# Performance work log

Hardware: AMD Instinct MI355X
Metric: run time of the kernel (lower is better)

Reference implementation:

```python
import jax, jax.numpy as jnp
import numpy as np

INPUT_DIM = 1024
EMBED_DIM = 256


def setup_inputs() -> dict:
    key = jax.random.key(0)
    ks = jax.random.split(key, 7)
    s_in = 1.0 / np.sqrt(INPUT_DIM)
    x = jax.random.normal(ks[0], (4, 2048, INPUT_DIM), dtype=jnp.float32)
    Wq = jax.random.uniform(ks[1], (INPUT_DIM, EMBED_DIM), jnp.float32, -s_in, s_in)
    bq = jax.random.uniform(ks[2], (EMBED_DIM,), jnp.float32, -s_in, s_in)
    Wk = jax.random.uniform(ks[3], (INPUT_DIM, EMBED_DIM), jnp.float32, -s_in, s_in)
    bk = jax.random.uniform(ks[4], (EMBED_DIM,), jnp.float32, -s_in, s_in)
    Wv = jax.random.uniform(ks[5], (INPUT_DIM, EMBED_DIM), jnp.float32, -s_in, s_in)
    bv = jax.random.uniform(ks[6], (EMBED_DIM,), jnp.float32, -s_in, s_in)
    return {"x": x, "Wq": Wq, "bq": bq, "Wk": Wk, "bk": bk, "Wv": Wv, "bv": bv}


def reference(x, Wq, bq, Wk, bk, Wv, bv):
    # B,T,C -> single-head attention. NOTE: original multiplies by C**0.5.
    C = x.shape[-1]
    scale = jnp.asarray(C, x.dtype) ** 0.5
    q = jnp.einsum('btc,ce->bte', x, Wq) + bq  # [B,T,E]
    k = jnp.einsum('btc,ce->bte', x, Wk) + bk
    v = jnp.einsum('btc,ce->bte', x, Wv) + bv
    wei = jnp.einsum('bqe,bke->bqk', q, k) * scale  # [B,T,T]
    wei = jax.nn.softmax(wei, axis=-1)
    # dropout p=0.0 (eval): identity
    out = jnp.einsum('bqk,bke->bqe', wei, v)  # [B,T,E]
    return out
```

## Files before the change

### kernel.cpp

```cpp
#include <hip/hip_runtime.h>
#include <math.h>

#define IDIM 1024
#define EDIM 256
#define NB 4
#define NT 2048
#define NROW 8192

typedef __attribute__((ext_vector_type(8))) short short8;
typedef __attribute__((ext_vector_type(4))) float f32x4;

#define MFMA16(A,B,C) __builtin_amdgcn_mfma_f32_16x16x32_bf16(A,B,C,0,0,0)
#define GLD16(gsrc, ldst) __builtin_amdgcn_global_load_lds( \
    (const __attribute__((address_space(1))) unsigned int*)(gsrc), \
    (__attribute__((address_space(3))) unsigned int*)(ldst), 16, 0, 0)

__device__ __forceinline__ unsigned short f2bf(float x){
    unsigned u = __builtin_bit_cast(unsigned, x);
    u += 0x7fffu + ((u >> 16) & 1u);
    return (unsigned short)(u >> 16);
}
__device__ __forceinline__ float bf2f(unsigned short h){
    unsigned u = ((unsigned)h) << 16;
    return __builtin_bit_cast(float, u);
}

__global__ __launch_bounds__(256) void split_w(
    const float* __restrict__ Wq, const float* __restrict__ Wk, const float* __restrict__ Wv,
    ushort* __restrict__ Wqh, ushort* __restrict__ Wql,
    ushort* __restrict__ Wkh, ushort* __restrict__ Wkl,
    ushort* __restrict__ Wvh)
{
    int u = blockIdx.x * 256 + threadIdx.x;
    int z   = u >> 15;
    int rem = u & 32767;
    int ko  = rem >> 8;
    int e   = rem & 255;
    const float* W = (z == 0) ? Wq : (z == 1) ? Wk : Wv;
    ushort* Oh = (z == 0) ? Wqh : (z == 1) ? Wkh : Wvh;
    ushort* Ol = (z == 0) ? Wql : Wkl;
    union { ushort us[8]; uint4 v; } hi, lo;
    #pragma unroll
    for (int j = 0; j < 8; ++j) {
        float wv = W[(size_t)(ko * 8 + j) * 256 + e];
        unsigned short h = f2bf(wv);
        hi.us[j] = h;
        lo.us[j] = f2bf(wv - bf2f(h));
    }
    *(uint4*)(Oh + (size_t)e * 1024 + ko * 8) = hi.v;
    if (z < 2) *(uint4*)(Ol + (size_t)e * 1024 + ko * 8) = lo.v;
}

__global__ __launch_bounds__(256, 3) void qkv_proj(
    const float* __restrict__ X,
    const ushort* __restrict__ Whq, const ushort* __restrict__ Wlq,
    const ushort* __restrict__ Whk, const ushort* __restrict__ Wlk,
    const ushort* __restrict__ Whv,
    const float* __restrict__ bq, const float* __restrict__ bk, const float* __restrict__ bv,
    ushort* __restrict__ Qh, ushort* __restrict__ Ql,
    ushort* __restrict__ Kh, ushort* __restrict__ Kl,
    ushort* __restrict__ Vt)
{
    __shared__ ushort Ah[259 * 8], Al[259 * 8];
    __shared__ ushort Bh[512 * 8], Bl[512 * 8];

    const int tid = threadIdx.x;
    const int lane = tid & 63, w = tid >> 6;
    const int ln = tid & 15, quad = (tid >> 4) & 3;
    const int z = blockIdx.z;
    const int n0 = blockIdx.x * 128, m0 = blockIdx.y * 64;
    const ushort* Wh = (z == 0) ? Whq : (z == 1) ? Whk : Whv;
    const ushort* Wl = (z == 0) ? Wlq : Wlk;

    f32x4 acc[4][2];
    #pragma unroll
    for (int mi = 0; mi < 4; ++mi)
        #pragma unroll
        for (int ni = 0; ni < 2; ++ni) acc[mi][ni] = (f32x4){0.f, 0.f, 0.f, 0.f};

    const int am = tid >> 2, ak8 = (tid & 3) * 8;
    const float* xp = X + (size_t)(m0 + am) * IDIM + ak8;
    const ushort* bsrc0 = Wh + (size_t)(n0 + lane) * IDIM + w * 8;
    const ushort* bsrc1 = Wh + (size_t)(n0 + 64 + lane) * IDIM + w * 8;
    const ushort* blsrc0 = Wl + (size_t)(n0 + lane) * IDIM + w * 8;
    const ushort* blsrc1 = Wl + (size_t)(n0 + 64 + lane) * IDIM + w * 8;
    ushort* bd0 = Bh + (size_t)(w * 128) * 8;
    ushort* bd1 = Bh + (size_t)(w * 128 + 64) * 8;
    ushort* bld0 = Bl + (size_t)(w * 128) * 8;
    ushort* bld1 = Bl + (size_t)(w * 128 + 64) * 8;

    for (int kk = 0; kk < IDIM; kk += 32) {
        GLD16(bsrc0 + kk, bd0);
        GLD16(bsrc1 + kk, bd1);
        if (z < 2) { GLD16(blsrc0 + kk, bld0); GLD16(blsrc1 + kk, bld1); }
        {
            float4 a0 = *(const float4*)(xp + kk);
            float4 a1 = *(const float4*)(xp + kk + 4);
            float xv[8] = {a0.x, a0.y, a0.z, a0.w, a1.x, a1.y, a1.z, a1.w};
            union { ushort us[8]; uint4 v; } hi, lo;
            #pragma unroll
            for (int j = 0; j < 8; ++j) {
                unsigned short hh = f2bf(xv[j]);
                hi.us[j] = hh;
                lo.us[j] = f2bf(xv[j] - bf2f(hh));
            }
            int unit = (tid & 3) * 65 + am;
            *(uint4*)(Ah + unit * 8) = hi.v;
            if (z < 2) *(uint4*)(Al + unit * 8) = lo.v;
        }
        __syncthreads();

        short8 ah[4], al4[4];
        #pragma unroll
        for (int mi = 0; mi < 4; ++mi) {
            int au = quad * 65 + mi * 16 + ln;
            ah[mi] = *(const short8*)(Ah + au * 8);
            if (z < 2) al4[mi] = *(const short8*)(Al + au * 8);
        }
        #pragma unroll
        for (int ni = 0; ni < 2; ++ni) {
            int bu = quad * 128 + w * 32 + ni * 16 + ln;
            short8 bh = *(const short8*)(Bh + bu * 8);
            if (z < 2) {
                short8 bl = *(const short8*)(Bl + bu * 8);
                #pragma unroll
                for (int mi = 0; mi < 4; ++mi) {
                    acc[mi][ni] = MFMA16(ah[mi], bh, acc[mi][ni]);
                    acc[mi][ni] = MFMA16(ah[mi], bl, acc[mi][ni]);
                    acc[mi][ni] = MFMA16(al4[mi], bh, acc[mi][ni]);
                }
            } else {
                #pragma unroll
                for (int mi = 0; mi < 4; ++mi)
                    acc[mi][ni] = MFMA16(ah[mi], bh, acc[mi][ni]);
            }
        }
        __syncthreads();
    }

    if (z < 2) {
        ushort* OH = (z == 0) ? Qh : Kh;
        ushort* OL = (z == 0) ? Ql : Kl;
        const float* bias = (z == 0) ? bq : bk;
        const float scale = (z == 0) ? 46.16624130844683f : 1.0f;
        #pragma unroll
        for (int ni = 0; ni < 2; ++ni) {
            int col = n0 + w * 32 + ni * 16 + ln;
            float bb = bias[col];
            #pragma unroll
            for (int mi = 0; mi < 4; ++mi)
                #pragma unroll
                for (int r = 0; r < 4; ++r) {
                    int row = m0 + mi * 16 + quad * 4 + r;
                    float v = (acc[mi][ni][r] + bb) * scale;
                    unsigned short hh = f2bf(v);
                    OH[(size_t)row * EDIM + col] = hh;
                    OL[(size_t)row * EDIM + col] = f2bf(v - bf2f(hh));
                }
        }
    } else {
        #pragma unroll
        for (int ni = 0; ni < 2; ++ni) {
            int col = n0 + w * 32 + ni * 16 + ln;
            float bb = bv[col];
            #pragma unroll
            for (int mi = 0; mi < 4; ++mi) {
                int rowb = m0 + mi * 16 + quad * 4;
                union { ushort us[4]; uint2 v; } pk;
                #pragma unroll
                for (int r = 0; r < 4; ++r) pk.us[r] = f2bf(acc[mi][ni][r] + bb);
                *(uint2*)(Vt + (size_t)col * NROW + rowb) = pk.v;
            }
        }
    }
}

__global__ __launch_bounds__(256, 2) void attn(
    const ushort* __restrict__ Qh, const ushort* __restrict__ Ql,
    const ushort* __restrict__ Kh, const ushort* __restrict__ Kl,
    const ushort* __restrict__ Vt, ushort* __restrict__ Op, float* __restrict__ mlbuf)
{
    __shared__ ushort KVbuf[4096];
    __shared__ ushort Qls[16384];
    __shared__ ushort Pall[4 * 1088];

    const int tid = threadIdx.x;
    const int lane = tid & 63;
    const int ln = tid & 15, quad = (tid >> 4) & 3, w = tid >> 6;
    ushort* Qls_w = Qls + w * 4096;
    ushort* Pw = Pall + w * 1088;

    const int id = blockIdx.x;
    const int cls = id & 15;
    const int b = cls >> 2, kvq = cls & 3;
    const int qt = id >> 4;
    const int qrow0w = b * NT + qt * 64 + w * 16;
    const int kvbase = b * NT + kvq * 512;

    short8 qh8[8];
    #pragma unroll
    for (int kc = 0; kc < 8; ++kc)
        qh8[kc] = *(const short8*)(Qh + (size_t)(qrow0w + ln) * EDIM + kc * 32 + quad * 8);
    #pragma unroll
    for (int i = 0; i < 8; ++i) {
        int u = i * 64 + lane;
        int ko = u >> 4, ln2 = u & 15;
        *(uint4*)(Qls_w + u * 8) =
            *(const uint4*)(Ql + (size_t)(qrow0w + ln2) * EDIM + ko * 8);
    }

    float m_r[4], l_r[4];
    #pragma unroll
    for (int r = 0; r < 4; ++r) { m_r[r] = -3e38f; l_r[r] = 0.f; }
    f32x4 o[16];
    #pragma unroll
    for (int ni = 0; ni < 16; ++ni) o[ni] = (f32x4){0.f, 0.f, 0.f, 0.f};

    for (int t = 0; t < 8; ++t) {
        const int kv0 = kvbase + t * 64;
        f32x4 s[4];
        #pragma unroll
        for (int ni = 0; ni < 4; ++ni) s[ni] = (f32x4){0.f, 0.f, 0.f, 0.f};

        #pragma unroll
        for (int kc = 0; kc < 8; ++kc) {
            size_t goff = (size_t)(kv0 + w * 16 + (lane & 15)) * EDIM
                          + kc * 32 + (lane >> 4) * 8;
            GLD16(Kh + goff, KVbuf + w * 512);
            GLD16(Kl + goff, KVbuf + 2048 + w * 512);
            __syncthreads();
            short8 ql8 = *(const short8*)(Qls_w + ((kc * 4 + quad) * 16 + ln) * 8);
            #pragma unroll
            for (int ni = 0; ni < 4; ++ni) {
                short8 bh = *(const short8*)(KVbuf + (ni * 64 + quad * 16 + ln) * 8);
                short8 bl = *(const short8*)(KVbuf + 2048 + (ni * 64 + quad * 16 + ln) * 8);
                s[ni] = MFMA16(qh8[kc], bh, s[ni]);
                s[ni] = MFMA16(qh8[kc], bl, s[ni]);
                s[ni] = MFMA16(ql8, bh, s[ni]);
            }
            __syncthreads();
        }

        float mt[4];
        #pragma unroll
        for (int r = 0; r < 4; ++r)
            mt[r] = fmaxf(fmaxf(s[0][r], s[1][r]), fmaxf(s[2][r], s[3][r]));
        #pragma unroll
        for (int mask = 1; mask < 16; mask <<= 1)
            #pragma unroll
            for (int r = 0; r < 4; ++r)
                mt[r] = fmaxf(mt[r], __shfl_xor(mt[r], mask));
        float alpha[4];
        #pragma unroll
        for (int r = 0; r < 4; ++r) {
            float mn = fmaxf(m_r[r], mt[r]);
            alpha[r] = exp2f(m_r[r] - mn);
            m_r[r] = mn;
        }
        float ls[4] = {0.f, 0.f, 0.f, 0.f};
        #pragma unroll
        for (int ni = 0; ni < 4; ++ni) {
            int colb = ni * 16 + ln;
            #pragma unroll
            for (int r = 0; r < 4; ++r) {
                float p = exp2f(s[ni][r] - m_r[r]);
                ls[r] += p;
                Pw[((colb >> 3) * 17 + quad * 4 + r) * 8 + (colb & 7)] = f2bf(p);
            }
        }
        #pragma unroll
        for (int mask = 1; mask < 16; mask <<= 1)
            #pragma unroll
            for (int r = 0; r < 4; ++r)
                ls[r] += __shfl_xor(ls[r], mask);
        #pragma unroll
        for (int r = 0; r < 4; ++r) l_r[r] = l_r[r] * alpha[r] + ls[r];
        #pragma unroll
        for (int ni = 0; ni < 16; ++ni)
            #pragma unroll
            for (int r = 0; r < 4; ++r) o[ni][r] *= alpha[r];

        short8 apk0 = *(const short8*)(Pw + (quad * 17 + ln) * 8);
        short8 apk1 = *(const short8*)(Pw + ((4 + quad) * 17 + ln) * 8);
        #pragma unroll
        for (int vs = 0; vs < 4; ++vs) {
            size_t gv = (size_t)(vs * 64 + w * 16 + (lane & 15)) * NROW
                        + kv0 + (lane >> 4) * 8;
            GLD16(Vt + gv, KVbuf + w * 1024);
            GLD16(Vt + gv + 32, KVbuf + w * 1024 + 512);
            __syncthreads();
            #pragma unroll
            for (int ni = 0; ni < 4; ++ni) {
                short8 v0 = *(const short8*)(KVbuf + (ni * 128 + quad * 16 + ln) * 8);
                short8 v1 = *(const short8*)(KVbuf + (ni * 128 + 64 + quad * 16 + ln) * 8);
                o[vs * 4 + ni] = MFMA16(apk0, v0, o[vs * 4 + ni]);
                o[vs * 4 + ni] = MFMA16(apk1, v1, o[vs * 4 + ni]);
            }
            __syncthreads();
        }
    }

    const int p = (b * 32 + qt) * 4 + kvq;
    if (ln == 0) {
        #pragma unroll
        for (int r = 0; r < 4; ++r) {
            int row = w * 16 + quad * 4 + r;
            *(float2*)(mlbuf + ((size_t)p * 64 + row) * 2) = make_float2(m_r[r], l_r[r]);
        }
    }
    #pragma unroll
    for (int ni = 0; ni < 16; ++ni)
        #pragma unroll
        for (int r = 0; r < 4; ++r) {
            int row = w * 16 + quad * 4 + r;
            Op[(size_t)p * 16384 + row * 256 + ni * 16 + ln] = f2bf(o[ni][r]);
        }
}

__global__ __launch_bounds__(256) void attn_merge(
    const ushort* __restrict__ Op, const float* __restrict__ mlbuf, float* __restrict__ out)
{
    const int bid = blockIdx.x, t = threadIdx.x;
    const int b = bid >> 7, qt = (bid >> 2) & 31, rg = bid & 3;
    const int row = rg * 16 + (t >> 4);
    const int e0 = (t & 15) * 16;
    const int pb = (b * 32 + qt) * 4;
    float mv[4], lv[4];
    float M = -3e38f;
    #pragma unroll
    for (int w2 = 0; w2 < 4; ++w2) {
        float2 ml = *(const float2*)(mlbuf + ((size_t)(pb + w2) * 64 + row) * 2);
        mv[w2] = ml.x; lv[w2] = ml.y;
        M = fmaxf(M, ml.x);
    }
    float sc[4], denom = 0.f;
    #pragma unroll
    for (int w2 = 0; w2 < 4; ++w2) {
        sc[w2] = exp2f(mv[w2] - M);
        denom += sc[w2] * lv[w2];
    }
    float inv = 1.0f / denom;
    #pragma unroll
    for (int w2 = 0; w2 < 4; ++w2) sc[w2] *= inv;

    float acc[16] = {};
    #pragma unroll
    for (int w2 = 0; w2 < 4; ++w2) {
        const ushort* src = Op + (size_t)(pb + w2) * 16384 + row * 256 + e0;
        #pragma unroll
        for (int c = 0; c < 2; ++c) {
            union { ushort us[8]; uint4 v; } u;
            u.v = *(const uint4*)(src + c * 8);
            #pragma unroll
            for (int j = 0; j < 8; ++j)
                acc[c * 8 + j] += sc[w2] * bf2f(u.us[j]);
        }
    }
    float* op = out + ((size_t)b * NT + qt * 64 + row) * EDIM + e0;
    #pragma unroll
    for (int g = 0; g < 4; ++g)
        *(float4*)(op + g * 4) = make_float4(acc[g*4], acc[g*4+1], acc[g*4+2], acc[g*4+3]);
}

extern "C" void kernel_launch(void* const* d_in, const int* in_sizes, int n_in,
                              void* d_out, int out_size, void* d_ws, size_t ws_size,
                              hipStream_t stream) {
    const float* x  = (const float*)d_in[0];
    const float* Wq = (const float*)d_in[1];
    const float* bq = (const float*)d_in[2];
    const float* Wk = (const float*)d_in[3];
    const float* bk = (const float*)d_in[4];
    const float* Wv = (const float*)d_in[5];
    const float* bv = (const float*)d_in[6];
    float* out = (float*)d_out;

    const size_t NE = (size_t)NB * NT * EDIM;
    ushort* Qh = (ushort*)d_ws;
    ushort* Ql = Qh + NE;
    ushort* Kh = Ql + NE;
    ushort* Kl = Kh + NE;
    ushort* Vt = Kl + NE;
    ushort* Wqh = Vt + NE;
    ushort* Wql = Wqh + 256 * 1024;
    ushort* Wkh = Wql + 256 * 1024;
    ushort* Wkl = Wkh + 256 * 1024;
    ushort* Wvh = Wkl + 256 * 1024;
    ushort* Op  = Wvh + 256 * 1024;
    float*  mlb = (float*)(Op + (size_t)512 * 16384);

    split_w<<<384, 256, 0, stream>>>(Wq, Wk, Wv, Wqh, Wql, Wkh, Wkl, Wvh);
    qkv_proj<<<dim3(2, 128, 3), 256, 0, stream>>>(x, Wqh, Wql, Wkh, Wkl, Wvh,
                                                  bq, bk, bv, Qh, Ql, Kh, Kl, Vt);
    attn<<<512, 256, 0, stream>>>(Qh, Ql, Kh, Kl, Vt, Op, mlb);
    attn_merge<<<512, 256, 0, stream>>>(Op, mlb, out);
}
```

Measured before the change: 212.8 us.

## Pre-split X into bf16 hi/lo and enlarge QKV projection tile to 128x128

Adds a split_x kernel that converts X once into bf16 high/low halves, instead of each of the six projection blocks per row tile reconverting fp32 X on the fly. qkv_proj now loads A through direct global-to-LDS loads like B, and uses a 128x128 tile with a 2x2 warp grid and 4x4 MFMA fragments per warp, which roughly halves grid size and improves operand reuse. The cost is an extra pass writing 32MB of bf16 X, more registers and lower occupancy, and Op/mlbuf now alias the Xh workspace region.

```diff
diff --git a/kernel.cpp b/kernel.cpp
--- a/kernel.cpp
+++ b/kernel.cpp
@@ -23,6 +23,24 @@
 __device__ __forceinline__ float bf2f(unsigned short h){
     unsigned u = ((unsigned)h) << 16;
     return __builtin_bit_cast(float, u);
+}
+
+__global__ __launch_bounds__(256) void split_x(
+    const float* __restrict__ X, ushort* __restrict__ Xh, ushort* __restrict__ Xl)
+{
+    size_t i = ((size_t)blockIdx.x * 256 + threadIdx.x) * 8;
+    float4 a = *(const float4*)(X + i);
+    float4 b = *(const float4*)(X + i + 4);
+    float v[8] = {a.x, a.y, a.z, a.w, b.x, b.y, b.z, b.w};
+    union { ushort us[8]; uint4 u; } hi, lo;
+    #pragma unroll
+    for (int j = 0; j < 8; ++j) {
+        unsigned short h = f2bf(v[j]);
+        hi.us[j] = h;
+        lo.us[j] = f2bf(v[j] - bf2f(h));
+    }
+    *(uint4*)(Xh + i) = hi.u;
+    *(uint4*)(Xl + i) = lo.u;
 }
 
 __global__ __launch_bounds__(256) void split_w(
@@ -51,8 +69,8 @@
     if (z < 2) *(uint4*)(Ol + (size_t)e * 1024 + ko * 8) = lo.v;
 }
 
-__global__ __launch_bounds__(256, 3) void qkv_proj(
-    const float* __restrict__ X,
+__global__ __launch_bounds__(256) void qkv_proj(
+    const ushort* __restrict__ Xh, const ushort* __restrict__ Xl,
     const ushort* __restrict__ Whq, const ushort* __restrict__ Wlq,
     const ushort* __restrict__ Whk, const ushort* __restrict__ Wlk,
     const ushort* __restrict__ Whv,
@@ -61,79 +79,81 @@
     ushort* __restrict__ Kh, ushort* __restrict__ Kl,
     ushort* __restrict__ Vt)
 {
-    __shared__ ushort Ah[259 * 8], Al[259 * 8];
-    __shared__ ushort Bh[512 * 8], Bl[512 * 8];
+    __shared__ ushort Ah[4096], Al[4096], Bh[4096], Bl[4096];
 
     const int tid = threadIdx.x;
     const int lane = tid & 63, w = tid >> 6;
     const int ln = tid & 15, quad = (tid >> 4) & 3;
+    const int wr = w >> 1, wc = w & 1;
     const int z = blockIdx.z;
-    const int n0 = blockIdx.x * 128, m0 = blockIdx.y * 64;
+    const int n0 = blockIdx.x * 128, m0 = blockIdx.y * 128;
     const ushort* Wh = (z == 0) ? Whq : (z == 1) ? Whk : Whv;
     const ushort* Wl = (z == 0) ? Wlq : Wlk;
 
-    f32x4 acc[4][2];
+    f32x4 acc[4][4];
     #pragma unroll
     for (int mi = 0; mi < 4; ++mi)
         #pragma unroll
-        for (int ni = 0; ni < 2; ++ni) acc[mi][ni] = (f32x4){0.f, 0.f, 0.f, 0.f};
-
-    const int am = tid >> 2, ak8 = (tid & 3) * 8;
-    const float* xp = X + (size_t)(m0 + am) * IDIM + ak8;
-    const ushort* bsrc0 = Wh + (size_t)(n0 + lane) * IDIM + w * 8;
-    const ushort* bsrc1 = Wh + (size_t)(n0 + 64 + lane) * IDIM + w * 8;
-    const ushort* blsrc0 = Wl + (size_t)(n0 + lane) * IDIM + w * 8;
-    const ushort* blsrc1 = Wl + (size_t)(n0 + 64 + lane) * IDIM + w * 8;
-    ushort* bd0 = Bh + (size_t)(w * 128) * 8;
-    ushort* bd1 = Bh + (size_t)(w * 128 + 64) * 8;
-    ushort* bld0 = Bl + (size_t)(w * 128) * 8;
-    ushort* bld1 = Bl + (size_t)(w * 128 + 64) * 8;
+        for (int ni = 0; ni < 4; ++ni) acc[mi][ni] = (f32x4){0.f, 0.f, 0.f, 0.f};
+
+    const ushort* a0 = Xh + (size_t)(m0 + lane) * IDIM + w * 8;
+    const ushort* a1 = Xh + (size_t)(m0 + 64 + lane) * IDIM + w * 8;
+    const ushort* a0l = Xl + (size_t)(m0 + lane) * IDIM + w * 8;
+    const ushort* a1l = Xl + (size_t)(m0 + 64 + lane) * IDIM + w * 8;
+    const ushort* b0 = Wh + (size_t)(n0 + lane) * IDIM + w * 8;
+    const ushort* b1 = Wh + (size_t)(n0 + 64 + lane) * IDIM + w * 8;
+    const ushort* b0l = Wl + (size_t)(n0 + lane) * IDIM + w * 8;
+    const ushort* b1l = Wl + (size_t)(n0 + 64 + lane) * IDIM + w * 8;
+    ushort* dA0 = Ah + (size_t)(w * 128) * 8;
+    ushort* dA1 = Ah + (size_t)(w * 128 + 64) * 8;
+    ushort* dA0l = Al + (size_t)(w * 128) * 8;
+    ushort* dA1l = Al + (size_t)(w * 128 + 64) * 8;
+    ushort* dB0 = Bh + (size_t)(w * 128) * 8;
+    ushort* dB1 = Bh + (size_t)(w * 128 + 64) * 8;
+    ushort* dB0l = Bl + (size_t)(w * 128) * 8;
+    ushort* dB1l = Bl + (size_t)(w * 128 + 64) * 8;
 
     for (int kk = 0; kk < IDIM; kk += 32) {
-        GLD16(bsrc0 + kk, bd0);
-        GLD16(bsrc1 + kk, bd1);
-        if (z < 2) { GLD16(blsrc0 + kk, bld0); GLD16(blsrc1 + kk, bld1); }
-        {
-            float4 a0 = *(const float4*)(xp + kk);
-            float4 a1 = *(const float4*)(xp + kk + 4);
-            float xv[8] = {a0.x, a0.y, a0.z, a0.w, a1.x, a1.y, a1.z, a1.w};
-            union { ushort us[8]; uint4 v; } hi, lo;
-            #pragma unroll
-            for (int j = 0; j < 8; ++j) {
-                unsigned short hh = f2bf(xv[j]);
-                hi.us[j] = hh;
-                lo.us[j] = f2bf(xv[j] - bf2f(hh));
-            }
-            int unit = (tid & 3) * 65 + am;
-            *(uint4*)(Ah + unit * 8) = hi.v;
-            if (z < 2) *(uint4*)(Al + unit * 8) = lo.v;
+        GLD16(a0 + kk, dA0);
+        GLD16(a1 + kk, dA1);
+        GLD16(b0 + kk, dB0);
+        GLD16(b1 + kk, dB1);
+        if (z < 2) {
+            GLD16(a0l + kk, dA0l);
+            GLD16(a1l + kk, dA1l);
+            GLD16(b0l + kk, dB0l);
+            GLD16(b1l + kk, dB1l);
         }
         __syncthreads();
 
-        short8 ah[4], al4[4];
+        short8 ah[4], al[4], bh[4], bl[4];
         #pragma unroll
         for (int mi = 0; mi < 4; ++mi) {
-            int au = quad * 65 + mi * 16 + ln;
+            int au = quad * 128 + wr * 64 + mi * 16 + ln;
             ah[mi] = *(const short8*)(Ah + au * 8);
-            if (z < 2) al4[mi] = *(const short8*)(Al + au * 8);
-        }
-        #pragma unroll
-        for (int ni = 0; ni < 2; ++ni) {
-            int bu = quad * 128 + w * 32 + ni * 16 + ln;
-            short8 bh = *(const short8*)(Bh + bu * 8);
-            if (z < 2) {
-                short8 bl = *(const short8*)(Bl + bu * 8);
+            if (z < 2) al[mi] = *(const short8*)(Al + au * 8);
+        }
+        #pragma unroll
+        for (int ni = 0; ni < 4; ++ni) {
+            int bu = quad * 128 + wc * 64 + ni * 16 + ln;
+            bh[ni] = *(const short8*)(Bh + bu * 8);
+            if (z < 2) bl[ni] = *(const short8*)(Bl + bu * 8);
+        }
+        if (z < 2) {
+            #pragma unroll
+            for (int ni = 0; ni < 4; ++ni)
                 #pragma unroll
                 for (int mi = 0; mi < 4; ++mi) {
-                    acc[mi][ni] = MFMA16(ah[mi], bh, acc[mi][ni]);
-                    acc[mi][ni] = MFMA16(ah[mi], bl, acc[mi][ni]);
-                    acc[mi][ni] = MFMA16(al4[mi], bh, acc[mi][ni]);
+                    acc[mi][ni] = MFMA16(ah[mi], bh[ni], acc[mi][ni]);
+                    acc[mi][ni] = MFMA16(ah[mi], bl[ni], acc[mi][ni]);
+                    acc[mi][ni] = MFMA16(al[mi], bh[ni], acc[mi][ni]);
                 }
-            } else {
+        } else {
+            #pragma unroll
+            for (int ni = 0; ni < 4; ++ni)
                 #pragma unroll
                 for (int mi = 0; mi < 4; ++mi)
-                    acc[mi][ni] = MFMA16(ah[mi], bh, acc[mi][ni]);
-            }
+                    acc[mi][ni] = MFMA16(ah[mi], bh[ni], acc[mi][ni]);
         }
         __syncthreads();
     }
@@ -144,14 +164,14 @@
         const float* bias = (z == 0) ? bq : bk;
         const float scale = (z == 0) ? 46.16624130844683f : 1.0f;
         #pragma unroll
-        for (int ni = 0; ni < 2; ++ni) {
-            int col = n0 + w * 32 + ni * 16 + ln;
+        for (int ni = 0; ni < 4; ++ni) {
+            int col = n0 + wc * 64 + ni * 16 + ln;
             float bb = bias[col];
             #pragma unroll
             for (int mi = 0; mi < 4; ++mi)
                 #pragma unroll
                 for (int r = 0; r < 4; ++r) {
-                    int row = m0 + mi * 16 + quad * 4 + r;
+                    int row = m0 + wr * 64 + mi * 16 + quad * 4 + r;
                     float v = (acc[mi][ni][r] + bb) * scale;
                     unsigned short hh = f2bf(v);
                     OH[(size_t)row * EDIM + col] = hh;
@@ -160,12 +180,12 @@
         }
     } else {
         #pragma unroll
-        for (int ni = 0; ni < 2; ++ni) {
-            int col = n0 + w * 32 + ni * 16 + ln;
+        for (int ni = 0; ni < 4; ++ni) {
+            int col = n0 + wc * 64 + ni * 16 + ln;
             float bb = bv[col];
             #pragma unroll
             for (int mi = 0; mi < 4; ++mi) {
-                int rowb = m0 + mi * 16 + quad * 4;
+                int rowb = m0 + wr * 64 + mi * 16 + quad * 4;
                 union { ushort us[4]; uint2 v; } pk;
                 #pragma unroll
                 for (int r = 0; r < 4; ++r) pk.us[r] = f2bf(acc[mi][ni][r] + bb);
@@ -374,8 +394,11 @@
     const float* bv = (const float*)d_in[6];
     float* out = (float*)d_out;
 
+    const size_t NX = (size_t)NROW * IDIM;
     const size_t NE = (size_t)NB * NT * EDIM;
-    ushort* Qh = (ushort*)d_ws;
+    ushort* Xh = (ushort*)d_ws;
+    ushort* Xl = Xh + NX;
+    ushort* Qh = Xl + NX;
     ushort* Ql = Qh + NE;
     ushort* Kh = Ql + NE;
     ushort* Kl = Kh + NE;
@@ -385,12 +408,13 @@
     ushort* Wkh = Wql + 256 * 1024;
     ushort* Wkl = Wkh + 256 * 1024;
     ushort* Wvh = Wkl + 256 * 1024;
-    ushort* Op  = Wvh + 256 * 1024;
-    float*  mlb = (float*)(Op + (size_t)512 * 16384);
-
+    ushort* Op  = Xh;
+    float*  mlb = (float*)(Xh + (size_t)512 * 16384);
+
+    split_x<<<4096, 256, 0, stream>>>(x, Xh, Xl);
     split_w<<<384, 256, 0, stream>>>(Wq, Wk, Wv, Wqh, Wql, Wkh, Wkl, Wvh);
-    qkv_proj<<<dim3(2, 128, 3), 256, 0, stream>>>(x, Wqh, Wql, Wkh, Wkl, Wvh,
-                                                  bq, bk, bv, Qh, Ql, Kh, Kl, Vt);
+    qkv_proj<<<dim3(2, 64, 3), 256, 0, stream>>>(Xh, Xl, Wqh, Wql, Wkh, Wkl, Wvh,
+                                                 bq, bk, bv, Qh, Ql, Kh, Kl, Vt);
     attn<<<512, 256, 0, stream>>>(Qh, Ql, Kh, Kl, Vt, Op, mlb);
     attn_merge<<<512, 256, 0, stream>>>(Op, mlb, out);
 }
```

Measured after the change: 233.7 us. 1.1x slower.
